# Kernel optimization log

Measured on AMD Instinct MI355X. Metric: run time of the kernel, lower is better.

Reference implementation:

```python
import jax, jax.numpy as jnp
import numpy as np

N = 50000      # nodes
E = 1600000    # message edges (avg degree 32)
EQ = 500000    # link-prediction query edges
IN, HID, OUT, FCH = 128, 128, 64, 256
ALPHA = 0.5


def setup_inputs() -> dict:
    key = jax.random.key(0)
    ks = jax.random.split(key, 8)
    def p(k, shape):
        fan_in = shape[0]
        return jax.random.normal(k, shape, jnp.float32) * (1.0 / np.sqrt(fan_in))
    return {
        "x": jax.random.normal(ks[0], (N, IN), jnp.float32),
        "edge_index": jax.random.randint(ks[1], (2, E), 0, N),
        "edge_label_index": jax.random.randint(ks[2], (2, EQ), 0, N),
        "W1": p(ks[3], (IN, HID)),  "b1": jnp.zeros((HID,), jnp.float32),
        "W2": p(ks[4], (HID, OUT)), "b2": jnp.zeros((OUT,), jnp.float32),
        "Wf1": p(ks[5], (IN, FCH)), "bf1": jnp.zeros((FCH,), jnp.float32),
        "Wf2": p(ks[6], (FCH, OUT)), "bf2": jnp.zeros((OUT,), jnp.float32),
    }


def reference(x, edge_index, edge_label_index, W1, b1, W2, b2, Wf1, bf1, Wf2, bf2):
    n = x.shape[0]
    # GCN self-loops + symmetric normalization (PyG GCNConv defaults)
    loop = jnp.arange(n)
    src = jnp.concatenate([edge_index[0], loop])
    dst = jnp.concatenate([edge_index[1], loop])
    deg = jax.ops.segment_sum(jnp.ones_like(dst, jnp.float32), dst, num_segments=n)
    dinv = jnp.where(deg > 0, jax.lax.rsqrt(deg), 0.0)
    norm = dinv[src] * dinv[dst]  # [E+N]

    def gcn(h, W, b):
        h = h @ W                                  # transform first (PyG order)
        msg = norm[:, None] * h[src]               # gather + scale per edge
        return jax.ops.segment_sum(msg, dst, num_segments=n) + b

    x_gcn = jax.nn.relu(gcn(x, W1, b1))
    x_gcn = gcn(x_gcn, W2, b2)
    x_fc = jax.nn.relu(x @ Wf1 + bf1) @ Wf2 + bf2
    z = x_gcn * (1.0 - ALPHA) + x_fc * ALPHA       # [N, OUT]
    # edge dot-product decode
    return jnp.sum(z[edge_label_index[0]] * z[edge_label_index[1]], axis=1)
```

## Files before the change

kernel.cpp:

```cpp
#include <hip/hip_runtime.h>

#define FIN   128
#define FHID  128
#define FOUT  64
#define FFC   256
#define CHUNK 4096
#define BKBITS 7
#define BKN   128
#define ECAP  4608

typedef __attribute__((ext_vector_type(8))) short          bf16x8;
typedef __attribute__((ext_vector_type(4))) float          f32x4;
typedef __attribute__((ext_vector_type(2))) float          f32x2;
typedef __attribute__((ext_vector_type(8))) unsigned short u16x8;

static __device__ __forceinline__ unsigned short f2bf(float f) {
    unsigned int u = __float_as_uint(f);
    u = (u + 0x7fffu + ((u >> 16) & 1u)) >> 16;
    return (unsigned short)u;
}
static __device__ __forceinline__ float bf2f(unsigned short s) {
    return __uint_as_float(((unsigned int)s) << 16);
}
static __device__ __forceinline__ void accum_fp8(float* acc, uint4 g) {
    f32x2 p;
    p = __builtin_amdgcn_cvt_pk_f32_fp8(g.x, false); acc[0]  += p.x; acc[1]  += p.y;
    p = __builtin_amdgcn_cvt_pk_f32_fp8(g.x, true);  acc[2]  += p.x; acc[3]  += p.y;
    p = __builtin_amdgcn_cvt_pk_f32_fp8(g.y, false); acc[4]  += p.x; acc[5]  += p.y;
    p = __builtin_amdgcn_cvt_pk_f32_fp8(g.y, true);  acc[6]  += p.x; acc[7]  += p.y;
    p = __builtin_amdgcn_cvt_pk_f32_fp8(g.z, false); acc[8]  += p.x; acc[9]  += p.y;
    p = __builtin_amdgcn_cvt_pk_f32_fp8(g.z, true);  acc[10] += p.x; acc[11] += p.y;
    p = __builtin_amdgcn_cvt_pk_f32_fp8(g.w, false); acc[12] += p.x; acc[13] += p.y;
    p = __builtin_amdgcn_cvt_pk_f32_fp8(g.w, true);  acc[14] += p.x; acc[15] += p.y;
}

__global__ __launch_bounds__(256) void binA_kernel(
    const int* __restrict__ src, const int* __restrict__ dst,
    int* __restrict__ bcur, unsigned int* __restrict__ ebuf, int E)
{
    __shared__ int hist[512];
    __shared__ int rstart[512];
    __shared__ int lcur[512];
    int t = threadIdx.x;
    hist[t] = 0; hist[t + 256] = 0; lcur[t] = 0; lcur[t + 256] = 0;
    __syncthreads();
    int e0 = blockIdx.x * CHUNK;
    int e1 = min(e0 + CHUNK, E);
    for (int e = e0 + t; e < e1; e += 256)
        atomicAdd(&hist[dst[e] >> BKBITS], 1);
    __syncthreads();
    if (hist[t])       rstart[t]       = atomicAdd(&bcur[t],       hist[t]);
    if (hist[t + 256]) rstart[t + 256] = atomicAdd(&bcur[t + 256], hist[t + 256]);
    __syncthreads();
    for (int e = e0 + t; e < e1; e += 256) {
        int s = src[e], d = dst[e];
        int b = d >> BKBITS;
        int pos = rstart[b] + atomicAdd(&lcur[b], 1);
        if (pos < ECAP)
            ebuf[(size_t)b * ECAP + pos] =
                ((unsigned)s << BKBITS) | ((unsigned)d & (BKN - 1));
    }
}

__global__ __launch_bounds__(256) void binB_kernel(
    const unsigned int* __restrict__ ebuf, const int* __restrict__ bcnt,
    int2* __restrict__ rp2, int* __restrict__ col, float* __restrict__ dinv,
    const float* __restrict__ x, unsigned char* __restrict__ xs,
    int N)
{
    __shared__ int cnt[128];
    __shared__ int tmp[256];
    __shared__ int ccur[128];
    __shared__ int scur[256];
    __shared__ float sdinv[128];
    __shared__ unsigned int skey[ECAP];
    int b = blockIdx.x;
    int t = threadIdx.x;
    size_t base = (size_t)b * ECAP;
    int ne = min(bcnt[b], ECAP);
    if (t < 128) cnt[t] = 0;
    scur[t] = 0;
    __syncthreads();
    for (int e = t; e < ne; e += 256) {
        unsigned int k = ebuf[base + e];
        atomicAdd(&cnt[k & (BKN - 1)], 1);
        atomicAdd(&scur[k >> 15], 1);
    }
    __syncthreads();
    int c = (t < 128) ? cnt[t] : 0;
    tmp[t] = c;
    __syncthreads();
    int acc = c;
    for (int off = 1; off < 128; off <<= 1) {
        int a = (t >= off) ? tmp[t - off] : 0;
        __syncthreads();
        acc += a; tmp[t] = acc;
        __syncthreads();
    }
    if (t < 128) {
        float di = rsqrtf((float)c + 1.0f);
        sdinv[t] = di;
        int node = b * BKN + t;
        int st = (int)base + acc - c;
        if (node < N) { dinv[node] = di; rp2[node] = make_int2(st, st + c); }
        ccur[t] = st;
    }
    __syncthreads();
    int sv = scur[t];
    tmp[t] = sv;
    __syncthreads();
    int sacc = sv;
    for (int off = 1; off < 256; off <<= 1) {
        int a = (t >= off) ? tmp[t - off] : 0;
        __syncthreads();
        sacc += a; tmp[t] = sacc;
        __syncthreads();
    }
    scur[t] = sacc - sv;
    __syncthreads();
    for (int e = t; e < ne; e += 256) {
        unsigned int k = ebuf[base + e];
        int pos = atomicAdd(&scur[k >> 15], 1);
        skey[pos] = k;
    }
    __syncthreads();
    for (int w = 0; w < ne; w += 256) {
        int e = w + t;
        if (e < ne) {
            unsigned int k = skey[e];
            int pos = atomicAdd(&ccur[k & (BKN - 1)], 1);
            col[pos] = (int)(k >> BKBITS);
        }
        __syncthreads();
    }
    int nl0 = t >> 3;
    int f0 = (t & 7) << 4;
    #pragma unroll
    for (int it = 0; it < 4; it++) {
        int nl = it * 32 + nl0;
        int gn = b * BKN + nl;
        if (gn >= N) continue;
        float d2 = sdinv[nl];
        const float* xr = x + (size_t)gn * FIN + f0;
        float4 va = *(const float4*)(xr);
        float4 vb = *(const float4*)(xr + 4);
        float4 vc = *(const float4*)(xr + 8);
        float4 vd = *(const float4*)(xr + 12);
        float f[16] = { va.x * d2, va.y * d2, va.z * d2, va.w * d2,
                        vb.x * d2, vb.y * d2, vb.z * d2, vb.w * d2,
                        vc.x * d2, vc.y * d2, vc.z * d2, vc.w * d2,
                        vd.x * d2, vd.y * d2, vd.z * d2, vd.w * d2 };
        uint4 w;
        w.x = 0; w.y = 0; w.z = 0; w.w = 0;
        w.x = __builtin_amdgcn_cvt_pk_fp8_f32(f[0],  f[1],  w.x, false);
        w.x = __builtin_amdgcn_cvt_pk_fp8_f32(f[2],  f[3],  w.x, true);
        w.y = __builtin_amdgcn_cvt_pk_fp8_f32(f[4],  f[5],  w.y, false);
        w.y = __builtin_amdgcn_cvt_pk_fp8_f32(f[6],  f[7],  w.y, true);
        w.z = __builtin_amdgcn_cvt_pk_fp8_f32(f[8],  f[9],  w.z, false);
        w.z = __builtin_amdgcn_cvt_pk_fp8_f32(f[10], f[11], w.z, true);
        w.w = __builtin_amdgcn_cvt_pk_fp8_f32(f[12], f[13], w.w, false);
        w.w = __builtin_amdgcn_cvt_pk_fp8_f32(f[14], f[15], w.w, true);
        *(uint4*)(xs + (size_t)gn * 128 + f0) = w;
    }
}

__global__ __launch_bounds__(256) void fc_fused_kernel(
    const float* __restrict__ X,
    const float* __restrict__ Wf1,
    const float* __restrict__ Wf2,
    const float* __restrict__ bias1, const float* __restrict__ bias2,
    float* __restrict__ C, int M)
{
    __shared__ __align__(16) unsigned short lds[32768];
    const int tid  = threadIdx.x;
    const int lane = tid & 63;
    const int wave = tid >> 6;
    const int m = lane & 15;
    const int q = lane >> 4;
    const int rowbase = blockIdx.x * 64 + wave * 16;
    const int row = rowbase + m;

    for (int i = tid; i < 4096; i += 256) {
        int sl = i >> 8, n = i & 255;
        u16x8 o;
        #pragma unroll
        for (int j = 0; j < 8; j++) o[j] = f2bf(Wf1[(sl * 8 + j) * 256 + n]);
        ((u16x8*)lds)[(n << 4) | (sl ^ (n & 7))] = o;
    }
    __syncthreads();

    f32x4 acc[16] = {};
    const float* arow = X + (size_t)row * FIN + q * 8;
    for (int k0 = 0; k0 < 128; k0 += 32) {
        bf16x8 a = {};
        if (row < M) {
            float4 a0 = *(const float4*)(arow + k0);
            float4 a1 = *(const float4*)(arow + k0 + 4);
            a[0] = (short)f2bf(a0.x); a[1] = (short)f2bf(a0.y);
            a[2] = (short)f2bf(a0.z); a[3] = (short)f2bf(a0.w);
            a[4] = (short)f2bf(a1.x); a[5] = (short)f2bf(a1.y);
            a[6] = (short)f2bf(a1.z); a[7] = (short)f2bf(a1.w);
        }
        int sl = q + (k0 >> 3);
        #pragma unroll
        for (int c = 0; c < 16; c++) {
            int cc = c * 16 + m;
            bf16x8 b = ((const bf16x8*)lds)[(cc << 4) | (sl ^ (cc & 7))];
            acc[c] = __builtin_amdgcn_mfma_f32_16x16x32_bf16(a, b, acc[c], 0, 0, 0);
        }
    }
    __syncthreads();

    for (int i = tid; i < 2048; i += 256) {
        int sl = i >> 6, n = i & 63;
        u16x8 o;
        #pragma unroll
        for (int j = 0; j < 8; j++) o[j] = f2bf(Wf2[(sl * 8 + j) * 64 + n]);
        ((u16x8*)lds)[2048 + ((n << 5) | (sl ^ (n & 7)))] = o;
    }
    #pragma unroll
    for (int c = 0; c < 16; c++) {
        int cc = c * 16 + m;
        float bv = bias1[cc];
        #pragma unroll
        for (int r = 0; r < 4; r++) {
            int rr = wave * 16 + q * 4 + r;
            float v = fmaxf(acc[c][r] + bv, 0.f);
            lds[rr * 256 + ((((cc >> 3) ^ (rr & 7)) << 3) | (cc & 7))] = f2bf(v);
        }
    }
    __syncthreads();

    f32x4 acc2[4] = {};
    {
        int rr = wave * 16 + m;
        for (int k0 = 0; k0 < 256; k0 += 32) {
            int sl = q + (k0 >> 3);
            bf16x8 a = ((const bf16x8*)lds)[(rr << 5) | (sl ^ (rr & 7))];
            #pragma unroll
            for (int c = 0; c < 4; c++) {
                int cc = c * 16 + m;
                bf16x8 b = ((const bf16x8*)lds)[2048 + ((cc << 5) | (sl ^ (cc & 7)))];
                acc2[c] = __builtin_amdgcn_mfma_f32_16x16x32_bf16(a, b, acc2[c], 0, 0, 0);
            }
        }
    }
    __syncthreads();

    constexpr int ROWB = 4 * 16 * 4 + 16;
    unsigned char* wbase = (unsigned char*)lds + wave * 16 * ROWB;
    #pragma unroll
    for (int c = 0; c < 4; c++) {
        int lc = c * 16 + m;
        float bv = bias2[lc];
        #pragma unroll
        for (int r = 0; r < 4; r++)
            ((float*)(wbase + (q * 4 + r) * ROWB))[lc] = acc2[c][r] + bv;
    }
    #pragma unroll
    for (int p = 0; p < 4; p++) {
        int r2 = p * 4 + (lane >> 4);
        int bo = (lane & 15) * 16;
        int gr = rowbase + r2;
        if (gr < M) {
            uint4 v = *(const uint4*)(wbase + r2 * ROWB + bo);
            *(uint4*)((unsigned char*)C + (size_t)gr * FOUT * 4 + bo) = v;
        }
    }
}

__global__ __launch_bounds__(256) void pull1_kernel(
    const unsigned char* __restrict__ xs, const int2* __restrict__ rp2,
    const int* __restrict__ col, const float* __restrict__ dinv,
    unsigned short* __restrict__ aggx, int N)
{
    int tid = threadIdx.x;
    int node = blockIdx.x * 32 + (tid >> 3);
    if (node >= N) return;
    int f0 = (tid & 7) << 4;
    const unsigned char* base = xs + f0;
    float acc[16] = {};
    accum_fp8(acc, *(const uint4*)(base + (size_t)node * 128));
    int2 se = rp2[node];
    int e = se.x, end = se.y;
    for (; e + 4 <= end; e += 4) {
        int s0 = col[e], s1 = col[e + 1], s2 = col[e + 2], s3 = col[e + 3];
        uint4 g0 = *(const uint4*)(base + (size_t)s0 * 128);
        uint4 g1 = *(const uint4*)(base + (size_t)s1 * 128);
        uint4 g2 = *(const uint4*)(base + (size_t)s2 * 128);
        uint4 g3 = *(const uint4*)(base + (size_t)s3 * 128);
        accum_fp8(acc, g0); accum_fp8(acc, g1);
        accum_fp8(acc, g2); accum_fp8(acc, g3);
    }
    for (; e < end; e++)
        accum_fp8(acc, *(const uint4*)(base + (size_t)col[e] * 128));
    float di = dinv[node];
    u16x8 o0, o1;
    #pragma unroll
    for (int j = 0; j < 8; j++) {
        o0[j] = f2bf(di * acc[j]);
        o1[j] = f2bf(di * acc[8 + j]);
    }
    *(u16x8*)(aggx + (size_t)node * FIN + f0)     = o0;
    *(u16x8*)(aggx + (size_t)node * FIN + f0 + 8) = o1;
}

__global__ __launch_bounds__(256) void gcn_kernel(
    const unsigned short* __restrict__ A,
    const float* __restrict__ W1,
    const float* __restrict__ W2,
    const float* __restrict__ bias1,
    const float* __restrict__ rowscale,
    unsigned short* __restrict__ C, int M)
{
    __shared__ __align__(16) unsigned short lds[24576];
    const int tid  = threadIdx.x;
    const int lane = tid & 63;
    const int wave = tid >> 6;
    const int m = lane & 15;
    const int q = lane >> 4;
    const int rowbase = blockIdx.x * 64 + wave * 16;
    const int row = rowbase + m;

    for (int i = tid; i < 2048; i += 256) {
        int sl = i >> 7, n = i & 127;
        u16x8 o;
        #pragma unroll
        for (int j = 0; j < 8; j++) o[j] = f2bf(W1[(sl * 8 + j) * 128 + n]);
        ((u16x8*)lds)[(n << 4) | (sl ^ (n & 7))] = o;
    }
    for (int i = tid; i < 1024; i += 256) {
        int sl = i >> 6, n = i & 63;
        u16x8 o;
        #pragma unroll
        for (int j = 0; j < 8; j++) o[j] = f2bf(W2[(sl * 8 + j) * 64 + n]);
        ((u16x8*)lds)[2048 + ((n << 4) | (sl ^ (n & 7)))] = o;
    }
    __syncthreads();

    f32x4 acc[8] = {};
    const unsigned short* arow = A + (size_t)row * FIN + q * 8;
    for (int k0 = 0; k0 < 128; k0 += 32) {
        bf16x8 a = {};
        if (row < M) a = *(const bf16x8*)(arow + k0);
        int sl = q + (k0 >> 3);
        #pragma unroll
        for (int c = 0; c < 8; c++) {
            int cc = c * 16 + m;
            bf16x8 b = ((const bf16x8*)lds)[(cc << 4) | (sl ^ (cc & 7))];
            acc[c] = __builtin_amdgcn_mfma_f32_16x16x32_bf16(a, b, acc[c], 0, 0, 0);
        }
    }
    __syncthreads();

    #pragma unroll
    for (int c = 0; c < 8; c++) {
        int cc = c * 16 + m;
        float bv = bias1[cc];
        #pragma unroll
        for (int r = 0; r < 4; r++) {
            int rr = wave * 16 + q * 4 + r;
            float v = fmaxf(acc[c][r] + bv, 0.f);
            lds[rr * 128 + ((((cc >> 3) ^ (rr & 7)) << 3) | (cc & 7))] = f2bf(v);
        }
    }
    __syncthreads();

    f32x4 acc2[4] = {};
    {
        int rr = wave * 16 + m;
        for (int k0 = 0; k0 < 128; k0 += 32) {
            int sl = q + (k0 >> 3);
            bf16x8 a = ((const bf16x8*)lds)[(rr << 4) | (sl ^ (rr & 7))];
            #pragma unroll
            for (int c = 0; c < 4; c++) {
                int cc = c * 16 + m;
                bf16x8 b = ((const bf16x8*)lds)[2048 + ((cc << 4) | (sl ^ (cc & 7)))];
                acc2[c] = __builtin_amdgcn_mfma_f32_16x16x32_bf16(a, b, acc2[c], 0, 0, 0);
            }
        }
    }
    float rs[4];
    #pragma unroll
    for (int r = 0; r < 4; r++) {
        int gr = rowbase + q * 4 + r;
        rs[r] = (gr < M) ? rowscale[gr] : 1.0f;
    }
    __syncthreads();

    constexpr int ROWB = 4 * 16 * 2 + 16;
    unsigned char* wbase = (unsigned char*)lds + wave * 16 * ROWB;
    #pragma unroll
    for (int c = 0; c < 4; c++) {
        int lc = c * 16 + m;
        #pragma unroll
        for (int r = 0; r < 4; r++)
            ((unsigned short*)(wbase + (q * 4 + r) * ROWB))[lc] =
                f2bf(acc2[c][r] * rs[r]);
    }
    #pragma unroll
    for (int p = 0; p < 2; p++) {
        int r2 = p * 8 + (lane >> 3);
        int bo = (lane & 7) * 16;
        int gr = rowbase + r2;
        if (gr < M) {
            uint4 v = *(const uint4*)(wbase + r2 * ROWB + bo);
            *(uint4*)((unsigned char*)C + (size_t)gr * FOUT * 2 + bo) = v;
        }
    }
}

__global__ __launch_bounds__(256) void pull2_kernel(
    const unsigned short* __restrict__ t2s, const int2* __restrict__ rp2,
    const int* __restrict__ col, const float* __restrict__ dinv,
    const float* __restrict__ xfc, const float* __restrict__ b2,
    unsigned short* __restrict__ zbf, int N)
{
    int tid = threadIdx.x;
    int node = blockIdx.x * 32 + (tid >> 3);
    if (node >= N) return;
    int f0 = (tid & 7) << 3;
    const unsigned short* base = t2s + f0;
    u16x8 own = *(const u16x8*)(base + (size_t)node * FOUT);
    float acc[8];
    #pragma unroll
    for (int j = 0; j < 8; j++) acc[j] = bf2f(own[j]);
    int2 se = rp2[node];
    int e = se.x, end = se.y;
    for (; e + 4 <= end; e += 4) {
        int s0 = col[e], s1 = col[e + 1], s2 = col[e + 2], s3 = col[e + 3];
        u16x8 v0 = *(const u16x8*)(base + (size_t)s0 * FOUT);
        u16x8 v1 = *(const u16x8*)(base + (size_t)s1 * FOUT);
        u16x8 v2 = *(const u16x8*)(base + (size_t)s2 * FOUT);
        u16x8 v3 = *(const u16x8*)(base + (size_t)s3 * FOUT);
        #pragma unroll
        for (int j = 0; j < 8; j++)
            acc[j] += (bf2f(v0[j]) + bf2f(v1[j])) + (bf2f(v2[j]) + bf2f(v3[j]));
    }
    for (; e < end; e++) {
        u16x8 v = *(const u16x8*)(base + (size_t)col[e] * FOUT);
        #pragma unroll
        for (int j = 0; j < 8; j++) acc[j] += bf2f(v[j]);
    }
    float di = dinv[node];
    float4 x0 = *(const float4*)(xfc + (size_t)node * FOUT + f0);
    float4 x1 = *(const float4*)(xfc + (size_t)node * FOUT + f0 + 4);
    float4 bb0 = *(const float4*)(b2 + f0);
    float4 bb1 = *(const float4*)(b2 + f0 + 4);
    float xf[8] = { x0.x, x0.y, x0.z, x0.w, x1.x, x1.y, x1.z, x1.w };
    float bv[8] = { bb0.x, bb0.y, bb0.z, bb0.w, bb1.x, bb1.y, bb1.z, bb1.w };
    u16x8 o;
    #pragma unroll
    for (int j = 0; j < 8; j++)
        o[j] = f2bf(0.5f * (di * acc[j] + bv[j]) + 0.5f * xf[j]);
    *(u16x8*)(zbf + (size_t)node * FOUT + f0) = o;
}

__global__ void decode_kernel(
    const unsigned short* __restrict__ zbf, const int* __restrict__ eli,
    float* __restrict__ out, int Q)
{
    int tid = blockIdx.x * blockDim.x + threadIdx.x;
    int q = tid >> 3;
    if (q >= Q) return;
    int lane = tid & 7;
    int a = eli[q];
    int b = eli[Q + q];
    u16x8 va = *(const u16x8*)(zbf + (size_t)a * FOUT + lane * 8);
    u16x8 vb = *(const u16x8*)(zbf + (size_t)b * FOUT + lane * 8);
    float s = 0.f;
    #pragma unroll
    for (int j = 0; j < 8; j++) s += bf2f(va[j]) * bf2f(vb[j]);
    s += __shfl_down(s, 4, 8);
    s += __shfl_down(s, 2, 8);
    s += __shfl_down(s, 1, 8);
    if (lane == 0) out[q] = s;
}

extern "C" void kernel_launch(void* const* d_in, const int* in_sizes, int n_in,
                              void* d_out, int out_size, void* d_ws, size_t ws_size,
                              hipStream_t stream)
{
    const float* x   = (const float*)d_in[0];
    const int*   ei  = (const int*)  d_in[1];
    const int*   eli = (const int*)  d_in[2];
    const float* W1  = (const float*)d_in[3];
    const float* b1  = (const float*)d_in[4];
    const float* W2  = (const float*)d_in[5];
    const float* b2  = (const float*)d_in[6];
    const float* Wf1 = (const float*)d_in[7];
    const float* bf1 = (const float*)d_in[8];
    const float* Wf2 = (const float*)d_in[9];
    const float* bf2 = (const float*)d_in[10];
    float* out = (float*)d_out;

    const int N = in_sizes[0] / FIN;
    const int E = in_sizes[1] / 2;
    const int Q = in_sizes[2] / 2;
    const int* src = ei;
    const int* dst = ei + E;
    const int NBK = (N + BKN - 1) >> BKBITS;
    const int NBA = (E + CHUNK - 1) / CHUNK;

    char* p = (char*)d_ws;
    float* dinv = (float*)p;             p += (size_t)N * 4;
    int2*  rp2  = (int2*)p;              p += (size_t)N * 8;
    int*   bcur = (int*)p;               p += 2048;
    float* xfc = (float*)p;              p += (size_t)N * FOUT * 4;
    unsigned char* xs = (unsigned char*)p;     p += (size_t)N * 128;
    unsigned int* ebuf = (unsigned int*)p;  p += (size_t)NBK * ECAP * 4;
    int*   col  = (int*)p;               p += (size_t)NBK * ECAP * 4;
    unsigned short* aggx = (unsigned short*)p; p += (size_t)N * FIN * 2;
    unsigned short* t2s  = (unsigned short*)p; p += (size_t)N * FOUT * 2;
    unsigned short* zbf  = (unsigned short*)p; p += (size_t)N * FOUT * 2;

    const int TB = 256;

    hipMemsetAsync(bcur, 0, 2048, stream);

    fc_fused_kernel<<<(N + 63) / 64, TB, 0, stream>>>(
        x, Wf1, Wf2, bf1, bf2, xfc, N);

    binA_kernel<<<NBA, TB, 0, stream>>>(src, dst, bcur, ebuf, E);

    binB_kernel<<<NBK, TB, 0, stream>>>(ebuf, bcur, rp2, col, dinv, x, xs, N);

    pull1_kernel<<<(N + 31) / 32, TB, 0, stream>>>(xs, rp2, col, dinv, aggx, N);

    gcn_kernel<<<(N + 63) / 64, TB, 0, stream>>>(
        aggx, W1, W2, b1, dinv, t2s, N);

    pull2_kernel<<<(N + 31) / 32, TB, 0, stream>>>(
        t2s, rp2, col, dinv, xfc, b2, zbf, N);

    {
        long total = (long)Q * 8;
        decode_kernel<<<(int)((total + TB - 1) / TB), TB, 0, stream>>>(
            zbf, eli, out, Q);
    }
}
```

Measured before the change: 260.3 us.

## Pre-convert weights to transposed bf16 once and hoist operand loads

Adds extra blocks to the binning kernel that convert W1, W2, Wf1 and Wf2 into transposed bf16 buffers in workspace. The FC and GCN matmul kernels can then copy weights into LDS as 16-byte vector loads, where before every block did strided fp32 loads and its own bf16 conversion. A-operand rows and per-node scalars (dinv, xfc, bias) are loaded before the LDS fill or gather loop so their latency overlaps. This adds a dependency on the binning kernel before the FC kernel and some workspace, but removes redundant per-block conversion work.

```diff
diff --git a/kernel.cpp b/kernel.cpp
--- a/kernel.cpp
+++ b/kernel.cpp
@@ -34,14 +34,35 @@
     p = __builtin_amdgcn_cvt_pk_f32_fp8(g.w, true);  acc[14] += p.x; acc[15] += p.y;
 }
 
-__global__ __launch_bounds__(256) void binA_kernel(
+__global__ __launch_bounds__(256) void binA_cvt_kernel(
     const int* __restrict__ src, const int* __restrict__ dst,
-    int* __restrict__ bcur, unsigned int* __restrict__ ebuf, int E)
-{
+    int* __restrict__ bcur, unsigned int* __restrict__ ebuf, int E, int NBA,
+    const float* __restrict__ W1, const float* __restrict__ W2,
+    const float* __restrict__ Wf1, const float* __restrict__ Wf2,
+    unsigned short* __restrict__ w1t, unsigned short* __restrict__ w2t,
+    unsigned short* __restrict__ wf1t, unsigned short* __restrict__ wf2t)
+{
+    int t = threadIdx.x;
+    if (blockIdx.x >= NBA) {
+        long i = (long)(blockIdx.x - NBA) * 256 + t;
+        if (i < 16384) {
+            int k = (int)i >> 7, n = (int)i & 127;
+            w1t[n * 128 + k] = f2bf(W1[i]);
+        } else if (i < 24576) {
+            int j = (int)i - 16384; int k = j >> 6, n = j & 63;
+            w2t[n * 128 + k] = f2bf(W2[j]);
+        } else if (i < 57344) {
+            int j = (int)i - 24576; int k = j >> 8, n = j & 255;
+            wf1t[n * 128 + k] = f2bf(Wf1[j]);
+        } else if (i < 73728) {
+            int j = (int)i - 57344; int k = j >> 6, n = j & 63;
+            wf2t[n * 256 + k] = f2bf(Wf2[j]);
+        }
+        return;
+    }
     __shared__ int hist[512];
     __shared__ int rstart[512];
     __shared__ int lcur[512];
-    int t = threadIdx.x;
     hist[t] = 0; hist[t + 256] = 0; lcur[t] = 0; lcur[t + 256] = 0;
     __syncthreads();
     int e0 = blockIdx.x * CHUNK;
@@ -166,8 +187,8 @@
 
 __global__ __launch_bounds__(256) void fc_fused_kernel(
     const float* __restrict__ X,
-    const float* __restrict__ Wf1,
-    const float* __restrict__ Wf2,
+    const unsigned short* __restrict__ B1T,
+    const unsigned short* __restrict__ B2T,
     const float* __restrict__ bias1, const float* __restrict__ bias2,
     float* __restrict__ C, int M)
 {
@@ -180,27 +201,34 @@
     const int rowbase = blockIdx.x * 64 + wave * 16;
     const int row = rowbase + m;
 
+    float4 av[8] = {};
+    {
+        const float* arow = X + (size_t)row * FIN + q * 8;
+        if (row < M) {
+            #pragma unroll
+            for (int kk = 0; kk < 4; kk++) {
+                av[2 * kk]     = *(const float4*)(arow + kk * 32);
+                av[2 * kk + 1] = *(const float4*)(arow + kk * 32 + 4);
+            }
+        }
+    }
+
+    #pragma unroll 4
     for (int i = tid; i < 4096; i += 256) {
-        int sl = i >> 8, n = i & 255;
-        u16x8 o;
-        #pragma unroll
-        for (int j = 0; j < 8; j++) o[j] = f2bf(Wf1[(sl * 8 + j) * 256 + n]);
-        ((u16x8*)lds)[(n << 4) | (sl ^ (n & 7))] = o;
+        int n = i >> 4, sl = i & 15;
+        ((u16x8*)lds)[(n << 4) | (sl ^ (n & 7))] = ((const u16x8*)B1T)[i];
     }
     __syncthreads();
 
     f32x4 acc[16] = {};
-    const float* arow = X + (size_t)row * FIN + q * 8;
     for (int k0 = 0; k0 < 128; k0 += 32) {
-        bf16x8 a = {};
-        if (row < M) {
-            float4 a0 = *(const float4*)(arow + k0);
-            float4 a1 = *(const float4*)(arow + k0 + 4);
-            a[0] = (short)f2bf(a0.x); a[1] = (short)f2bf(a0.y);
-            a[2] = (short)f2bf(a0.z); a[3] = (short)f2bf(a0.w);
-            a[4] = (short)f2bf(a1.x); a[5] = (short)f2bf(a1.y);
-            a[6] = (short)f2bf(a1.z); a[7] = (short)f2bf(a1.w);
-        }
+        int kk = k0 >> 5;
+        float4 a0 = av[2 * kk], a1 = av[2 * kk + 1];
+        bf16x8 a;
+        a[0] = (short)f2bf(a0.x); a[1] = (short)f2bf(a0.y);
+        a[2] = (short)f2bf(a0.z); a[3] = (short)f2bf(a0.w);
+        a[4] = (short)f2bf(a1.x); a[5] = (short)f2bf(a1.y);
+        a[6] = (short)f2bf(a1.z); a[7] = (short)f2bf(a1.w);
         int sl = q + (k0 >> 3);
         #pragma unroll
         for (int c = 0; c < 16; c++) {
@@ -211,12 +239,10 @@
     }
     __syncthreads();
 
+    #pragma unroll 2
     for (int i = tid; i < 2048; i += 256) {
-        int sl = i >> 6, n = i & 63;
-        u16x8 o;
-        #pragma unroll
-        for (int j = 0; j < 8; j++) o[j] = f2bf(Wf2[(sl * 8 + j) * 64 + n]);
-        ((u16x8*)lds)[2048 + ((n << 5) | (sl ^ (n & 7)))] = o;
+        int n = i >> 5, sl = i & 31;
+        ((u16x8*)lds)[2048 + ((n << 5) | (sl ^ (n & 7)))] = ((const u16x8*)B2T)[i];
     }
     #pragma unroll
     for (int c = 0; c < 16; c++) {
@@ -279,9 +305,10 @@
     if (node >= N) return;
     int f0 = (tid & 7) << 4;
     const unsigned char* base = xs + f0;
+    float di = dinv[node];
+    int2 se = rp2[node];
     float acc[16] = {};
     accum_fp8(acc, *(const uint4*)(base + (size_t)node * 128));
-    int2 se = rp2[node];
     int e = se.x, end = se.y;
     for (; e + 4 <= end; e += 4) {
         int s0 = col[e], s1 = col[e + 1], s2 = col[e + 2], s3 = col[e + 3];
@@ -294,7 +321,6 @@
     }
     for (; e < end; e++)
         accum_fp8(acc, *(const uint4*)(base + (size_t)col[e] * 128));
-    float di = dinv[node];
     u16x8 o0, o1;
     #pragma unroll
     for (int j = 0; j < 8; j++) {
@@ -307,8 +333,8 @@
 
 __global__ __launch_bounds__(256) void gcn_kernel(
     const unsigned short* __restrict__ A,
-    const float* __restrict__ W1,
-    const float* __restrict__ W2,
+    const unsigned short* __restrict__ B1T,
+    const unsigned short* __restrict__ B2T,
     const float* __restrict__ bias1,
     const float* __restrict__ rowscale,
     unsigned short* __restrict__ C, int M)
@@ -322,27 +348,31 @@
     const int rowbase = blockIdx.x * 64 + wave * 16;
     const int row = rowbase + m;
 
+    bf16x8 areg[4] = {};
+    {
+        const unsigned short* arow = A + (size_t)row * FIN + q * 8;
+        if (row < M) {
+            #pragma unroll
+            for (int kk = 0; kk < 4; kk++)
+                areg[kk] = *(const bf16x8*)(arow + kk * 32);
+        }
+    }
+
+    #pragma unroll 2
     for (int i = tid; i < 2048; i += 256) {
-        int sl = i >> 7, n = i & 127;
-        u16x8 o;
-        #pragma unroll
-        for (int j = 0; j < 8; j++) o[j] = f2bf(W1[(sl * 8 + j) * 128 + n]);
-        ((u16x8*)lds)[(n << 4) | (sl ^ (n & 7))] = o;
-    }
+        int n = i >> 4, sl = i & 15;
+        ((u16x8*)lds)[(n << 4) | (sl ^ (n & 7))] = ((const u16x8*)B1T)[i];
+    }
+    #pragma unroll 2
     for (int i = tid; i < 1024; i += 256) {
-        int sl = i >> 6, n = i & 63;
-        u16x8 o;
-        #pragma unroll
-        for (int j = 0; j < 8; j++) o[j] = f2bf(W2[(sl * 8 + j) * 64 + n]);
-        ((u16x8*)lds)[2048 + ((n << 4) | (sl ^ (n & 7)))] = o;
+        int n = i >> 4, sl = i & 15;
+        ((u16x8*)lds)[2048 + ((n << 4) | (sl ^ (n & 7)))] = ((const u16x8*)B2T)[i];
     }
     __syncthreads();
 
     f32x4 acc[8] = {};
-    const unsigned short* arow = A + (size_t)row * FIN + q * 8;
     for (int k0 = 0; k0 < 128; k0 += 32) {
-        bf16x8 a = {};
-        if (row < M) a = *(const bf16x8*)(arow + k0);
+        bf16x8 a = areg[k0 >> 5];
         int sl = q + (k0 >> 3);
         #pragma unroll
         for (int c = 0; c < 8; c++) {
@@ -421,6 +451,11 @@
     if (node >= N) return;
     int f0 = (tid & 7) << 3;
     const unsigned short* base = t2s + f0;
+    float di = dinv[node];
+    float4 x0 = *(const float4*)(xfc + (size_t)node * FOUT + f0);
+    float4 x1 = *(const float4*)(xfc + (size_t)node * FOUT + f0 + 4);
+    float4 bb0 = *(const float4*)(b2 + f0);
+    float4 bb1 = *(const float4*)(b2 + f0 + 4);
     u16x8 own = *(const u16x8*)(base + (size_t)node * FOUT);
     float acc[8];
     #pragma unroll
@@ -442,11 +477,6 @@
         #pragma unroll
         for (int j = 0; j < 8; j++) acc[j] += bf2f(v[j]);
     }
-    float di = dinv[node];
-    float4 x0 = *(const float4*)(xfc + (size_t)node * FOUT + f0);
-    float4 x1 = *(const float4*)(xfc + (size_t)node * FOUT + f0 + 4);
-    float4 bb0 = *(const float4*)(b2 + f0);
-    float4 bb1 = *(const float4*)(b2 + f0 + 4);
     float xf[8] = { x0.x, x0.y, x0.z, x0.w, x1.x, x1.y, x1.z, x1.w };
     float bv[8] = { bb0.x, bb0.y, bb0.z, bb0.w, bb1.x, bb1.y, bb1.z, bb1.w };
     u16x8 o;
@@ -501,11 +531,16 @@
     const int* dst = ei + E;
     const int NBK = (N + BKN - 1) >> BKBITS;
     const int NBA = (E + CHUNK - 1) / CHUNK;
+    const int NCV = 73728 / 256;
 
     char* p = (char*)d_ws;
     float* dinv = (float*)p;             p += (size_t)N * 4;
     int2*  rp2  = (int2*)p;              p += (size_t)N * 8;
     int*   bcur = (int*)p;               p += 2048;
+    unsigned short* w1t  = (unsigned short*)p; p += FIN * FHID * 2;
+    unsigned short* w2t  = (unsigned short*)p; p += FHID * FOUT * 2;
+    unsigned short* wf1t = (unsigned short*)p; p += FIN * FFC * 2;
+    unsigned short* wf2t = (unsigned short*)p; p += FFC * FOUT * 2;
     float* xfc = (float*)p;              p += (size_t)N * FOUT * 4;
     unsigned char* xs = (unsigned char*)p;     p += (size_t)N * 128;
     unsigned int* ebuf = (unsigned int*)p;  p += (size_t)NBK * ECAP * 4;
@@ -518,17 +553,19 @@
 
     hipMemsetAsync(bcur, 0, 2048, stream);
 
+    binA_cvt_kernel<<<NBA + NCV, TB, 0, stream>>>(
+        src, dst, bcur, ebuf, E, NBA,
+        W1, W2, Wf1, Wf2, w1t, w2t, wf1t, wf2t);
+
     fc_fused_kernel<<<(N + 63) / 64, TB, 0, stream>>>(
-        x, Wf1, Wf2, bf1, bf2, xfc, N);
-
-    binA_kernel<<<NBA, TB, 0, stream>>>(src, dst, bcur, ebuf, E);
+        x, wf1t, wf2t, bf1, bf2, xfc, N);
 
     binB_kernel<<<NBK, TB, 0, stream>>>(ebuf, bcur, rp2, col, dinv, x, xs, N);
 
     pull1_kernel<<<(N + 31) / 32, TB, 0, stream>>>(xs, rp2, col, dinv, aggx, N);
 
     gcn_kernel<<<(N + 63) / 64, TB, 0, stream>>>(
-        aggx, W1, W2, b1, dinv, t2s, N);
+        aggx, w1t, w2t, b1, dinv, t2s, N);
 
     pull2_kernel<<<(N + 31) / 32, TB, 0, stream>>>(
         t2s, rp2, col, dinv, xfc, b2, zbf, N);
```

New measurement: 255.4 us. No clear change (-1.9%).
